# Kernel tuning notes

Hardware: AMD Instinct MI355X
Metric: run time of the kernel (lower is better)

The kernel has to match this reference:

```python
import jax, jax.numpy as jnp
import numpy as np

N_LAYERS, HEADS, D_IN, D_OUT, T, D, DFF = 4, 8, 16, 3, 1024, 512, 2048
D_HEAD = D // HEADS


def sinusoidal_pos_enc(t, d):
    # Faithful to the source: base = pos / 10000**(emb_idx/d); sin on even cols, cos on odd cols
    pos = jnp.arange(t, dtype=jnp.float32)[:, None]
    emb = jnp.arange(d, dtype=jnp.float32)[None, :]
    base = pos / jnp.power(10000.0, emb / d)
    even = (jnp.arange(d) % 2 == 0)[None, :]
    return jnp.where(even, jnp.sin(base), jnp.cos(base))  # (t, d)


def layer_norm(x, g, b, eps=1e-5):
    m = x.mean(-1, keepdims=True)
    v = ((x - m) ** 2).mean(-1, keepdims=True)
    return (x - m) / jnp.sqrt(v + eps) * g + b


def setup_inputs() -> dict:
    key = jax.random.key(0)
    ks = iter(jax.random.split(key, 24))
    s = 0.02
    inp = {}
    inp['x'] = jax.random.normal(next(ks), (16, T, D_IN), dtype=jnp.float32)
    inp['pad_mask'] = jax.random.randint(next(ks), (16, T), 0, 2, dtype=jnp.int32)
    inp['enc_W'] = jax.random.normal(next(ks), (D_IN, D), dtype=jnp.float32) * s
    inp['enc_b'] = jnp.zeros((D,), jnp.float32)
    for name in ['Wq', 'Wk', 'Wv', 'Wo']:
        inp[name] = jax.random.normal(next(ks), (N_LAYERS, D, D), dtype=jnp.float32) * s
    inp['ff_W1'] = jax.random.normal(next(ks), (N_LAYERS, D, DFF), dtype=jnp.float32) * s
    inp['ff_b1'] = jnp.zeros((N_LAYERS, DFF), jnp.float32)
    inp['ff_W2'] = jax.random.normal(next(ks), (N_LAYERS, DFF, D), dtype=jnp.float32) * s
    inp['ff_b2'] = jnp.zeros((N_LAYERS, D), jnp.float32)
    inp['ln1_g'] = jnp.ones((N_LAYERS, D), jnp.float32)
    inp['ln1_b'] = jnp.zeros((N_LAYERS, D), jnp.float32)
    inp['ln2_g'] = jnp.ones((N_LAYERS, D), jnp.float32)
    inp['ln2_b'] = jnp.zeros((N_LAYERS, D), jnp.float32)
    inp['out_W'] = jax.random.normal(next(ks), (D * T, D_OUT), dtype=jnp.float32) * s
    inp['out_b'] = jnp.zeros((D_OUT,), jnp.float32)
    return inp


def reference(x, enc_W, enc_b, Wq, Wk, Wv, Wo, ff_W1, ff_b1, ff_W2, ff_b2,
              ln1_g, ln1_b, ln2_g, ln2_b, out_W, out_b, pad_mask):
    n, t = x.shape[0], x.shape[1]
    # InputEncoding (linear) scaled by sqrt(d_model)
    h = (x @ enc_W + enc_b) * jnp.sqrt(jnp.float32(D))
    # Sinusoidal positional encoding, zeroed at masked (pad_mask==0) timesteps
    pe = sinusoidal_pos_enc(t, D)[None]  # (1, t, d)
    pe = jnp.where(pad_mask[..., None] == 0, 0.0, pe)  # (n, t, d)
    h = h + pe
    mask4 = (pad_mask[..., None, None] == 0)  # (n, t, 1, 1)
    for i in range(N_LAYERS):
        # --- MultiHeadAttention (faithful to source's transpose quirk) ---
        Qh = (h @ Wq[i]).reshape(n, t, HEADS, D_HEAD).swapaxes(2, 3)  # (n,t,dh,H)
        Kh = (h @ Wk[i]).reshape(n, t, HEADS, D_HEAD)                 # (n,t,H,dh)
        Vh = (h @ Wv[i]).reshape(n, t, HEADS, D_HEAD).swapaxes(2, 3)  # (n,t,dh,H)
        # energy: per-timestep (dh x dh), scaled by d_head**1/2 == d_head/2 (source precedence)
        energy = jnp.matmul(Qh, Kh) / (D_HEAD / 2.0)                  # (n,t,dh,dh)
        energy = jnp.where(mask4, -1e20, energy)
        attn = jax.nn.softmax(energy, axis=-1)
        head = jnp.matmul(attn, Vh)                                   # (n,t,dh,H)
        out = head.reshape(n, t, D) @ Wo[i]
        # residual + layer norm
        h = layer_norm(out + h, ln1_g[i], ln1_b[i])
        # --- FFN (relu) ---
        ff = jax.nn.relu(h @ ff_W1[i] + ff_b1[i]) @ ff_W2[i] + ff_b2[i]
        h = layer_norm(ff + h, ln2_g[i], ln2_b[i])
    # mode='train': flatten and project
    return h.reshape(n, -1) @ out_W + out_b  # (n, d_output)
```

## Files before the change

### kernel.cpp

```cpp
#include <hip/hip_runtime.h>
#include <cmath>

#define NB 16
#define TSEQ 1024
#define DIN 16
#define DM 512
#define DFFN 2048
#define NLAYERS 4
#define DOUTN 3
#define ROWS (NB*TSEQ)

typedef unsigned short u16;
typedef unsigned int   u32;
typedef short bf16x8 __attribute__((ext_vector_type(8)));
typedef u16   u16x4  __attribute__((ext_vector_type(4)));
typedef float f32x4  __attribute__((ext_vector_type(4)));

__device__ __forceinline__ float b2f(u16 v) { return __uint_as_float((unsigned)v << 16); }
__device__ __forceinline__ u16 f2b(float f) {
    unsigned u = __float_as_uint(f);
    return (u16)((u + 0x7FFFu + ((u >> 16) & 1u)) >> 16);
}

#define GLL(gp, lp) __builtin_amdgcn_global_load_lds( \
    (const __attribute__((address_space(1))) unsigned int*)(gp), \
    (__attribute__((address_space(3))) unsigned int*)(lp), 16, 0, 0)

template<int PERM>
__global__ __launch_bounds__(256) void transpose_cast(
    const float* __restrict__ in, u16* __restrict__ out,
    int K, int N, size_t in_lstride, size_t out_lstride)
{
    in  += (size_t)blockIdx.z * in_lstride;
    out += (size_t)blockIdx.z * out_lstride;
    __shared__ float t[32][33];
    int bk = blockIdx.x * 32, bn = blockIdx.y * 32;
    int x = threadIdx.x & 31, y = threadIdx.x >> 5;
    #pragma unroll
    for (int i = 0; i < 32; i += 8)
        t[y + i][x] = in[(size_t)(bk + y + i) * N + bn + x];
    __syncthreads();
    #pragma unroll
    for (int i = 0; i < 32; i += 8) {
        int row = bn + y + i;
        if (PERM) row = ((row & 63) << 3) | ((row >> 6) & 7);
        out[(size_t)row * K + bk + x] = f2b(t[x][y + i]);
    }
}

__global__ __launch_bounds__(128) void encode_kernel(
    const float* __restrict__ x, const int* __restrict__ pad,
    const float* __restrict__ W, const float* __restrict__ b,
    u16* __restrict__ h)
{
    int row = blockIdx.x;
    int t   = row & (TSEQ - 1);
    int c   = threadIdx.x * 4;
    float acc[4];
    #pragma unroll
    for (int j = 0; j < 4; ++j) acc[j] = b[c + j];
    const float* xr = x + (size_t)row * DIN;
    #pragma unroll
    for (int k = 0; k < DIN; ++k) {
        float xv = xr[k];
        const float* wr = W + (size_t)k * DM + c;
        #pragma unroll
        for (int j = 0; j < 4; ++j) acc[j] += xv * wr[j];
    }
    const float s = 22.62741699796952f;
    bool has_pe = (pad[row] != 0);
    u16x4 o;
    #pragma unroll
    for (int j = 0; j < 4; ++j) {
        acc[j] *= s;
        if (has_pe) {
            int d = c + j;
            float base = (float)t * powf(10000.0f, -(float)d * (1.0f/512.0f));
            acc[j] += ((d & 1) == 0) ? sinf(base) : cosf(base);
        }
        o[j] = f2b(acc[j]);
    }
    *(u16x4*)&h[(size_t)row * DM + c] = o;
}

template<int BIAS, int RELU>
__global__ __launch_bounds__(512, 8) void gemm_bf16(
    const u16* __restrict__ A, const u16* __restrict__ Bt,
    const float* __restrict__ bias, u16* __restrict__ C,
    int M, int N, int K)
{
    __shared__ u16 S[4][4096];
    const int tid  = threadIdx.x;
    const int lane = tid & 63;
    const int wid  = tid >> 6;
    const int wr   = wid >> 2;
    const int wc   = wid & 3;

    const int NY  = N >> 7;
    const int nwg = gridDim.x;
    const int cpx = nwg >> 3;
    const int bid = blockIdx.x;
    const int swz = (bid & 7) * cpx + (bid >> 3);
    const int bm  = (swz / NY) * 128;
    const int bn  = (swz % NY) * 128;

    const int srow   = tid >> 2;
    const int schunk = (tid & 3) ^ ((srow >> 1) & 3);
    const u16* Ag = A  + (size_t)(bm + srow) * K + schunk * 8;
    const u16* Bg = Bt + (size_t)(bn + srow) * K + schunk * 8;

    f32x4 acc[4][2];
    #pragma unroll
    for (int m = 0; m < 4; ++m)
        #pragma unroll
        for (int n = 0; n < 2; ++n)
            acc[m][n] = (f32x4){0.f, 0.f, 0.f, 0.f};

    const int fr  = lane & 15;
    const int grp = lane >> 4;

    auto STAGE = [&](int k0, int d) {
        GLL(Ag + k0, &S[d * 2 + 0][0] + tid * 8);
        GLL(Bg + k0, &S[d * 2 + 1][0] + tid * 8);
    };

    STAGE(0, 0);
    __syncthreads();

    int cur = 0;
    for (int k0 = 0; k0 < K; k0 += 32) {
        if (k0 + 32 < K) STAGE(k0 + 32, cur ^ 1);
        const u16* As = S[cur * 2 + 0];
        const u16* Bs = S[cur * 2 + 1];
        bf16x8 a[4], b[2];
        #pragma unroll
        for (int m = 0; m < 4; ++m) {
            int row = wr * 64 + m * 16 + fr;
            int slot = grp ^ ((row >> 1) & 3);
            a[m] = *(const bf16x8*)(As + row * 32 + slot * 8);
        }
        #pragma unroll
        for (int n = 0; n < 2; ++n) {
            int row = wc * 32 + n * 16 + fr;
            int slot = grp ^ ((row >> 1) & 3);
            b[n] = *(const bf16x8*)(Bs + row * 32 + slot * 8);
        }
        #pragma unroll
        for (int n = 0; n < 2; ++n)
            #pragma unroll
            for (int m = 0; m < 4; ++m)
                acc[m][n] = __builtin_amdgcn_mfma_f32_16x16x32_bf16(a[m], b[n], acc[m][n], 0, 0, 0);
        __syncthreads();
        cur ^= 1;
    }

    float bb[2] = {0.f, 0.f};
    if (BIAS) {
        #pragma unroll
        for (int n = 0; n < 2; ++n) bb[n] = bias[bn + wc * 32 + n * 16 + fr];
    }
    #pragma unroll
    for (int m = 0; m < 4; ++m) {
        #pragma unroll
        for (int n = 0; n < 2; ++n) {
            int col = bn + wc * 32 + n * 16 + fr;
            #pragma unroll
            for (int j = 0; j < 4; ++j) {
                int row = bm + wr * 64 + m * 16 + grp * 4 + j;
                float v = acc[m][n][j];
                if (BIAS) v += bb[n];
                if (RELU) v = fmaxf(v, 0.f);
                C[(size_t)row * N + col] = f2b(v);
            }
        }
    }
}

__global__ __launch_bounds__(256) void attn_mfma(
    const u16* __restrict__ QKV, const int* __restrict__ pad,
    u16* __restrict__ O)
{
    constexpr int WLDS = 2560;
    __shared__ u16 sh[4 * WLDS];
    const int wid  = threadIdx.x >> 6;
    const int lane = threadIdx.x & 63;
    const int site = blockIdx.x * 4 + wid;
    u16* P2 = sh + wid * WLDS;
    u16* Ol = P2 + 2048;

    const u16* base = QKV + (size_t)site * 1536;
    const int fr  = lane & 15;
    const int grp = lane >> 4;
    const bf16x8 zb = {0,0,0,0,0,0,0,0};
    const f32x4  zf = {0.f,0.f,0.f,0.f};

    if (pad[site] == 0) {
        bf16x8 vv = *(const bf16x8*)(base + 1024 + lane * 8);
        float s = 0.f;
        #pragma unroll
        for (int j = 0; j < 8; ++j) s += b2f((u16)vv[j]);
        s += __shfl_xor(s, 1); s += __shfl_xor(s, 2); s += __shfl_xor(s, 4);
        s *= (1.0f / 64.0f);
        bf16x8 ov;
        #pragma unroll
        for (int h2 = 0; h2 < 8; ++h2) ov[h2] = (short)f2b(__shfl(s, h2 * 8));
        *(bf16x8*)(O + (size_t)site * DM + lane * 8) = ov;
        return;
    }

    bf16x8 kt[4];
    #pragma unroll
    for (int n = 0; n < 4; ++n)
        kt[n] = (grp == 0) ? *(const bf16x8*)(base + 512 + (n * 16 + fr) * 8) : zb;
    bf16x8 bv[2];
    #pragma unroll
    for (int ks = 0; ks < 2; ++ks)
        bv[ks] = (fr < 8) ? *(const bf16x8*)(base + 1024 + fr * 64 + ks * 32 + grp * 8) : zb;

    const int swz = (fr & 3) ^ (fr >> 2);
    u16x4 pk23[4][2];

    #pragma unroll
    for (int m = 0; m < 4; ++m) {
        bf16x8 aq = (grp == 0) ? *(const bf16x8*)(base + (m * 16 + fr) * 8) : zb;
        f32x4 ev[4];
        #pragma unroll
        for (int n = 0; n < 4; ++n)
            ev[n] = __builtin_amdgcn_mfma_f32_16x16x32_bf16(kt[n], aq, zf, 0, 0, 0);
        f32x4 t0, t1;
        #pragma unroll
        for (int j = 0; j < 4; ++j) { t0[j] = fmaxf(ev[0][j], ev[1][j]); t1[j] = fmaxf(ev[2][j], ev[3][j]); }
        float mx = -1e30f;
        #pragma unroll
        for (int j = 0; j < 4; ++j) mx = fmaxf(mx, fmaxf(t0[j], t1[j]));
        mx = fmaxf(mx, __shfl_xor(mx, 16));
        mx = fmaxf(mx, __shfl_xor(mx, 32));
        float p[4][4];
        float s = 0.f;
        #pragma unroll
        for (int n = 0; n < 4; ++n)
            #pragma unroll
            for (int j = 0; j < 4; ++j) {
                p[n][j] = __expf((ev[n][j] - mx) * 0.03125f);
                s += p[n][j];
            }
        s += __shfl_xor(s, 16);
        s += __shfl_xor(s, 32);
        float inv = 1.0f / s;
        u16x4 pk[4];
        #pragma unroll
        for (int n = 0; n < 4; ++n)
            #pragma unroll
            for (int j = 0; j < 4; ++j) pk[n][j] = f2b(p[n][j] * inv);
        int row = m * 16 + fr;
        #pragma unroll
        for (int n = 0; n < 2; ++n) {
            int chunk = (n * 2 + (grp >> 1)) ^ swz;
            *(u16x4*)(P2 + row * 32 + chunk * 8 + (grp & 1) * 4) = pk[n];
        }
        pk23[m][0] = pk[2];
        pk23[m][1] = pk[3];
    }

    f32x4 pv[4];
    #pragma unroll
    for (int m = 0; m < 4; ++m) {
        int row = m * 16 + fr;
        bf16x8 ap = *(const bf16x8*)(P2 + row * 32 + ((grp ^ swz) * 8));
        pv[m] = __builtin_amdgcn_mfma_f32_16x16x32_bf16(ap, bv[0], zf, 0, 0, 0);
    }
    asm volatile("s_waitcnt lgkmcnt(0)" ::: "memory");
    __builtin_amdgcn_sched_barrier(0);

    #pragma unroll
    for (int m = 0; m < 4; ++m) {
        int row = m * 16 + fr;
        #pragma unroll
        for (int n = 0; n < 2; ++n) {
            int chunk = (n * 2 + (grp >> 1)) ^ swz;
            *(u16x4*)(P2 + row * 32 + chunk * 8 + (grp & 1) * 4) = pk23[m][n];
        }
    }
    #pragma unroll
    for (int m = 0; m < 4; ++m) {
        int row = m * 16 + fr;
        bf16x8 ap = *(const bf16x8*)(P2 + row * 32 + ((grp ^ swz) * 8));
        pv[m] = __builtin_amdgcn_mfma_f32_16x16x32_bf16(ap, bv[1], pv[m], 0, 0, 0);
    }

    #pragma unroll
    for (int m = 0; m < 4; ++m)
        #pragma unroll
        for (int j = 0; j < 4; ++j) {
            int row = m * 16 + grp * 4 + j;
            if (fr < 8) Ol[row * 8 + fr] = f2b(pv[m][j]);
        }
    __syncthreads();
    bf16x8 o = *(const bf16x8*)(Ol + lane * 8);
    *(bf16x8*)(O + (size_t)site * DM + lane * 8) = o;
}

__global__ __launch_bounds__(256) void add_ln_kernel(
    const u16* __restrict__ A, u16* __restrict__ H,
    const float* __restrict__ g, const float* __restrict__ b)
{
    int row  = blockIdx.x * 4 + (threadIdx.x >> 6);
    int lane = threadIdx.x & 63;
    const u16* a = A + (size_t)row * DM + lane * 8;
    u16* h = H + (size_t)row * DM + lane * 8;
    bf16x8 av = *(const bf16x8*)a;
    bf16x8 hv = *(const bf16x8*)h;
    float v[8];
    float s = 0.f;
    #pragma unroll
    for (int j = 0; j < 8; ++j) { v[j] = b2f((u16)av[j]) + b2f((u16)hv[j]); s += v[j]; }
    #pragma unroll
    for (int off = 32; off > 0; off >>= 1) s += __shfl_xor(s, off, 64);
    float mean = s * (1.0f / 512.0f);
    float var = 0.f;
    #pragma unroll
    for (int j = 0; j < 8; ++j) { float d = v[j] - mean; var += d * d; }
    #pragma unroll
    for (int off = 32; off > 0; off >>= 1) var += __shfl_xor(var, off, 64);
    float rstd = rsqrtf(var * (1.0f / 512.0f) + 1e-5f);
    bf16x8 ov;
    #pragma unroll
    for (int j = 0; j < 8; ++j) {
        int d = lane * 8 + j;
        ov[j] = (short)f2b((v[j] - mean) * rstd * g[d] + b[d]);
    }
    *(bf16x8*)h = ov;
}

__global__ __launch_bounds__(256) void out_stage1(
    const u16* __restrict__ h, const float* __restrict__ W,
    float* __restrict__ partial)
{
    int b = blockIdx.x, s = blockIdx.y;
    int tid = threadIdx.x;
    const u16* hb = h + (size_t)b * (TSEQ * DM) + (size_t)s * 8192;
    const float* Wb = W + (size_t)s * 8192 * 3;
    float a0 = 0.f, a1 = 0.f, a2 = 0.f;
    #pragma unroll 4
    for (int it = 0; it < 32; ++it) {
        int i = it * 256 + tid;
        float hv = b2f(hb[i]);
        a0 += hv * Wb[i * 3 + 0];
        a1 += hv * Wb[i * 3 + 1];
        a2 += hv * Wb[i * 3 + 2];
    }
    __shared__ float red[3][256];
    red[0][tid] = a0; red[1][tid] = a1; red[2][tid] = a2;
    __syncthreads();
    for (int off = 128; off > 0; off >>= 1) {
        if (tid < off) {
            red[0][tid] += red[0][tid + off];
            red[1][tid] += red[1][tid + off];
            red[2][tid] += red[2][tid + off];
        }
        __syncthreads();
    }
    if (tid == 0) {
        partial[(b * 64 + s) * 3 + 0] = red[0][0];
        partial[(b * 64 + s) * 3 + 1] = red[1][0];
        partial[(b * 64 + s) * 3 + 2] = red[2][0];
    }
}

__global__ __launch_bounds__(64) void out_stage2(
    const float* __restrict__ partial, const float* __restrict__ ob,
    float* __restrict__ out)
{
    int t = threadIdx.x;
    if (t < NB * DOUTN) {
        int b = t / 3, o = t % 3;
        float s = ob[o];
        for (int k = 0; k < 64; ++k) s += partial[(b * 64 + k) * 3 + o];
        out[t] = s;
    }
}

extern "C" void kernel_launch(void* const* d_in, const int* in_sizes, int n_in,
                              void* d_out, int out_size, void* d_ws, size_t ws_size,
                              hipStream_t stream)
{
    const float* x    = (const float*)d_in[0];
    const int*   pad  = (const int*)  d_in[1];
    const float* encW = (const float*)d_in[2];
    const float* encB = (const float*)d_in[3];
    const float* Wq   = (const float*)d_in[4];
    const float* Wk   = (const float*)d_in[5];
    const float* Wv   = (const float*)d_in[6];
    const float* Wo   = (const float*)d_in[7];
    const float* fW1  = (const float*)d_in[8];
    const float* fb1  = (const float*)d_in[9];
    const float* fW2  = (const float*)d_in[10];
    const float* fb2  = (const float*)d_in[11];
    const float* l1g  = (const float*)d_in[12];
    const float* l1b  = (const float*)d_in[13];
    const float* l2g  = (const float*)d_in[14];
    const float* l2b  = (const float*)d_in[15];
    const float* outW = (const float*)d_in[16];
    const float* outB = (const float*)d_in[17];
    float* out = (float*)d_out;

    const size_t WL  = 3145728;
    const size_t BUF = (size_t)ROWS * DM;
    const size_t need = (4 * WL + 6 * BUF) * sizeof(u16);
    if (ws_size < need) return;
    u16* wt = (u16*)d_ws;
    u16* h  = wt + 4 * WL;
    u16* b0 = h  + BUF;
    u16* b3 = b0 + 3 * BUF;
    u16* b4 = b3 + BUF;

    transpose_cast<1><<<dim3(16,16,4), 256, 0, stream>>>(Wq,  wt + 0,       512,  512,  (size_t)512*512,  WL);
    transpose_cast<1><<<dim3(16,16,4), 256, 0, stream>>>(Wk,  wt + 262144,  512,  512,  (size_t)512*512,  WL);
    transpose_cast<0><<<dim3(16,16,4), 256, 0, stream>>>(Wv,  wt + 524288,  512,  512,  (size_t)512*512,  WL);
    transpose_cast<0><<<dim3(16,16,4), 256, 0, stream>>>(Wo,  wt + 786432,  512,  512,  (size_t)512*512,  WL);
    transpose_cast<0><<<dim3(16,64,4), 256, 0, stream>>>(fW1, wt + 1048576, 512,  2048, (size_t)512*2048, WL);
    transpose_cast<0><<<dim3(64,16,4), 256, 0, stream>>>(fW2, wt + 2097152, 2048, 512,  (size_t)2048*512, WL);

    encode_kernel<<<ROWS, 128, 0, stream>>>(x, pad, encW, encB, h);

    for (int l = 0; l < NLAYERS; ++l) {
        u16* wl = wt + (size_t)l * WL;
        gemm_bf16<0,0><<<dim3((ROWS/128)*(1536/128)), 512, 0, stream>>>(h, wl, nullptr, b0, ROWS, 1536, DM);
        attn_mfma<<<ROWS/4, 256, 0, stream>>>(b0, pad, b3);
        gemm_bf16<0,0><<<dim3((ROWS/128)*(DM/128)), 512, 0, stream>>>(b3, wl + 786432, nullptr, b4, ROWS, DM, DM);
        add_ln_kernel<<<ROWS/4, 256, 0, stream>>>(b4, h, l1g + l*DM, l1b + l*DM);
        gemm_bf16<1,1><<<dim3((ROWS/128)*(DFFN/128)), 512, 0, stream>>>(h, wl + 1048576, fb1 + (size_t)l*DFFN, b0, ROWS, DFFN, DM);
        gemm_bf16<1,0><<<dim3((ROWS/128)*(DM/128)), 512, 0, stream>>>(b0, wl + 2097152, fb2 + (size_t)l*DM, b4, ROWS, DM, DFFN);
        add_ln_kernel<<<ROWS/4, 256, 0, stream>>>(b4, h, l2g + l*DM, l2b + l*DM);
    }

    out_stage1<<<dim3(NB, 64), 256, 0, stream>>>(h, outW, (float*)b0);
    out_stage2<<<1, 64, 0, stream>>>((float*)b0, outB, out);
}
```

Measured before the change: 792.6 us.

## Triple-buffer GEMM LDS staging with explicit vmcnt waits and single barrier

The bf16 GEMM moves from a double-buffered LDS pipeline with two __syncthreads per k-step to a three-stage ring. Two tiles are prefetched ahead, and each step uses an explicit s_waitcnt vmcnt plus one s_barrier. LDS reads become inline-asm ds_read_b128 with an lgkmcnt wait before the MFMAs. The aim is to hide global-to-LDS latency and cut barrier overhead, at the cost of more LDS per block (launch bounds drop to 6 waves/SIMD) and fragile hand-managed wait counts.

```diff
diff --git a/kernel.cpp b/kernel.cpp
--- a/kernel.cpp
+++ b/kernel.cpp
@@ -26,6 +26,20 @@
     (const __attribute__((address_space(1))) unsigned int*)(gp), \
     (__attribute__((address_space(3))) unsigned int*)(lp), 16, 0, 0)
 
+typedef __attribute__((address_space(3))) const u16 lds_cu16;
+__device__ __forceinline__ bf16x8 ds_read16(const u16* p) {
+    bf16x8 r;
+    asm volatile("ds_read_b128 %0, %1" : "=v"(r) : "v"((lds_cu16*)p));
+    return r;
+}
+
+#define WAITVM2() asm volatile("s_waitcnt vmcnt(2)" ::: "memory")
+#define WAITVM0() asm volatile("s_waitcnt vmcnt(0)" ::: "memory")
+#define WAITLGKM0() do { asm volatile("s_waitcnt lgkmcnt(0)" ::: "memory"); \
+                         __builtin_amdgcn_sched_barrier(0); } while (0)
+#define BARR() do { asm volatile("" ::: "memory"); __builtin_amdgcn_s_barrier(); \
+                    asm volatile("" ::: "memory"); } while (0)
+
 template<int PERM>
 __global__ __launch_bounds__(256) void transpose_cast(
     const float* __restrict__ in, u16* __restrict__ out,
@@ -84,12 +98,12 @@
 }
 
 template<int BIAS, int RELU>
-__global__ __launch_bounds__(512, 8) void gemm_bf16(
+__global__ __launch_bounds__(512, 6) void gemm_bf16(
     const u16* __restrict__ A, const u16* __restrict__ Bt,
     const float* __restrict__ bias, u16* __restrict__ C,
     int M, int N, int K)
 {
-    __shared__ u16 S[4][4096];
+    __shared__ u16 S[3][2][4096];
     const int tid  = threadIdx.x;
     const int lane = tid & 63;
     const int wid  = tid >> 6;
@@ -119,39 +133,40 @@
     const int fr  = lane & 15;
     const int grp = lane >> 4;
 
-    auto STAGE = [&](int k0, int d) {
-        GLL(Ag + k0, &S[d * 2 + 0][0] + tid * 8);
-        GLL(Bg + k0, &S[d * 2 + 1][0] + tid * 8);
+    auto STAGE = [&](int kt, int d) {
+        GLL(Ag + (size_t)kt * 32, &S[d][0][0] + tid * 8);
+        GLL(Bg + (size_t)kt * 32, &S[d][1][0] + tid * 8);
     };
 
+    const int nt = K >> 5;
     STAGE(0, 0);
-    __syncthreads();
-
-    int cur = 0;
-    for (int k0 = 0; k0 < K; k0 += 32) {
-        if (k0 + 32 < K) STAGE(k0 + 32, cur ^ 1);
-        const u16* As = S[cur * 2 + 0];
-        const u16* Bs = S[cur * 2 + 1];
+    STAGE(1, 1);
+
+    for (int it = 0; it < nt; ++it) {
+        if (it + 1 < nt) { WAITVM2(); } else { WAITVM0(); }
+        BARR();
+        if (it + 2 < nt) STAGE(it + 2, (it + 2) % 3);
+        const u16* As = &S[it % 3][0][0];
+        const u16* Bs = &S[it % 3][1][0];
         bf16x8 a[4], b[2];
         #pragma unroll
         for (int m = 0; m < 4; ++m) {
             int row = wr * 64 + m * 16 + fr;
             int slot = grp ^ ((row >> 1) & 3);
-            a[m] = *(const bf16x8*)(As + row * 32 + slot * 8);
+            a[m] = ds_read16(As + row * 32 + slot * 8);
         }
         #pragma unroll
         for (int n = 0; n < 2; ++n) {
             int row = wc * 32 + n * 16 + fr;
             int slot = grp ^ ((row >> 1) & 3);
-            b[n] = *(const bf16x8*)(Bs + row * 32 + slot * 8);
-        }
+            b[n] = ds_read16(Bs + row * 32 + slot * 8);
+        }
+        WAITLGKM0();
         #pragma unroll
         for (int n = 0; n < 2; ++n)
             #pragma unroll
             for (int m = 0; m < 4; ++m)
                 acc[m][n] = __builtin_amdgcn_mfma_f32_16x16x32_bf16(a[m], b[n], acc[m][n], 0, 0, 0);
-        __syncthreads();
-        cur ^= 1;
     }
 
     float bb[2] = {0.f, 0.f};
```

Result: no change. 803.7 us (+1.4%).
